# Kernel tuning notes

Measured on AMD Instinct MI355X. Metric: run time of the kernel, lower is better.

The kernel has to match this reference:

```python
import jax, jax.numpy as jnp
import numpy as np

# Fixed architecture constants from the source
B, T, D, V, L, H = 4096, 128, 64, 65, 3, 8
HD = D // H  # head_size = 8
DF = 4 * D   # 256


def _layernorm(x, g, b, eps=1e-5):
    mu = jnp.mean(x, axis=-1, keepdims=True)
    var = jnp.mean(jnp.square(x - mu), axis=-1, keepdims=True)
    return (x - mu) * jax.lax.rsqrt(var + eps) * g + b


def setup_inputs() -> dict:
    key = jax.random.key(0)
    ks = iter(jax.random.split(key, 64))
    s = 0.02
    n = lambda shape: jax.random.normal(next(ks), shape, dtype=jnp.float32) * s
    inp = {
        "tok_emb": n((V, D)),
        "pos_emb": n((T, D)),
        # per-block params stacked on leading layer dim L=3
        "ln1_g": jnp.ones((L, D), jnp.float32), "ln1_b": jnp.zeros((L, D), jnp.float32),
        "wq": n((L, D, D)), "wk": n((L, D, D)), "wv": n((L, D, D)),
        "wo": n((L, D, D)), "bo": jnp.zeros((L, D), jnp.float32),
        "ln2_g": jnp.ones((L, D), jnp.float32), "ln2_b": jnp.zeros((L, D), jnp.float32),
        "w1": n((L, D, DF)), "b1": jnp.zeros((L, DF), jnp.float32),
        "w2": n((L, DF, D)), "b2": jnp.zeros((L, D), jnp.float32),
        "lnf_g": jnp.ones((D,), jnp.float32), "lnf_b": jnp.zeros((D,), jnp.float32),
        "lm_w": n((D, V)), "lm_b": jnp.zeros((V,), jnp.float32),
        "idx": jax.random.randint(next(ks), (B, T), 0, V),
        "targets": jax.random.randint(next(ks), (B, T), 0, V),
    }
    return inp


def _forward(tok_emb, pos_emb, ln1_g, ln1_b, wq, wk, wv, wo, bo,
             ln2_g, ln2_b, w1, b1, w2, b2, lnf_g, lnf_b, lm_w, lm_b,
             idx, targets):
    b, t = idx.shape
    x = tok_emb[idx] + pos_emb[:t]  # [B,T,D]
    mask = jnp.tril(jnp.ones((t, t), bool))
    scale = 1.0 / np.sqrt(HD)
    for l in range(L):  # 3 structurally identical blocks (dropout = identity at eval)
        xn = _layernorm(x, ln1_g[l], ln1_b[l])
        # 8 per-head projections fused into one [D,D] matmul (concat along out dim)
        q = (xn @ wq[l]).reshape(b, t, H, HD)
        k = (xn @ wk[l]).reshape(b, t, H, HD)
        v = (xn @ wv[l]).reshape(b, t, H, HD)
        scores = jnp.einsum('bqhd,bkhd->bhqk', q, k) * scale
        scores = jnp.where(mask, scores, -jnp.inf)
        probs = jax.nn.softmax(scores, axis=-1)
        attn = jnp.einsum('bhqk,bkhd->bqhd', probs, v).reshape(b, t, D)
        x = x + attn @ wo[l] + bo[l]
        xn = _layernorm(x, ln2_g[l], ln2_b[l])
        x = x + jax.nn.relu(xn @ w1[l] + b1[l]) @ w2[l] + b2[l]
    x = _layernorm(x, lnf_g, lnf_b)
    logits = (x @ lm_w + lm_b).reshape(b * t, V)
    logp = jax.nn.log_softmax(logits, axis=-1)
    loss = -jnp.mean(jnp.take_along_axis(logp, targets.reshape(b * t, 1), axis=1))
    return logits, loss


def reference(tok_emb, pos_emb, ln1_g, ln1_b, wq, wk, wv, wo, bo,
              ln2_g, ln2_b, w1, b1, w2, b2, lnf_g, lnf_b, lm_w, lm_b,
              idx, targets):
    return _forward(tok_emb, pos_emb, ln1_g, ln1_b, wq, wk, wv, wo, bo,
                    ln2_g, ln2_b, w1, b1, w2, b2, lnf_g, lnf_b, lm_w, lm_b,
                    idx, targets)
```

## Files before the change

kernel.cpp:

```cpp
#include <hip/hip_runtime.h>
#include <hip/hip_bf16.h>

#define NB  4096
#define NT  128
#define ND  64
#define NV  65
#define NL  3
#define NH  8
#define NDF 256
#define NBT (NB*NT)

#define OFF_TOK   0
#define OFF_POS   4160
#define OFF_LN1G  12352
#define OFF_LN1B  12544
#define OFF_WQ    12736
#define OFF_WK    25024
#define OFF_WV    37312
#define OFF_WO    49600
#define OFF_BO    61888
#define OFF_LN2G  62080
#define OFF_LN2B  62272
#define OFF_W1    62464
#define OFF_B1    111616
#define OFF_W2    112384
#define OFF_B2    161536
#define OFF_LNFG  161728
#define OFF_LNFB  161792
#define OFF_LMW   161856
#define OFF_LMB   166016
#define CVT_TOTAL 166081
#define OFF_LOSS  166144
#define OFF_FLAG  166145

#define PKF       166148
#define PK_ELEMS  147456
#define NEED_WS   ((size_t)(PKF + PK_ELEMS) * 4)

typedef short s8v  __attribute__((ext_vector_type(8)));
typedef float f4v  __attribute__((ext_vector_type(4)));

struct CvtArgs { const void* p[19]; };

__device__ __forceinline__ unsigned short f2bf(float x) {
    unsigned int u = __float_as_uint(x);
    u = (u + 0x7fffu + ((u >> 16) & 1u)) >> 16;
    return (unsigned short)u;
}
__device__ __forceinline__ float bf2f(unsigned short h) {
    return __uint_as_float(((unsigned int)h) << 16);
}
__device__ __forceinline__ f4v mfma16(s8v a, s8v b, f4v c) {
    return __builtin_amdgcn_mfma_f32_16x16x32_bf16(a, b, c, 0, 0, 0);
}

__global__ void diag_fill(float* __restrict__ out, int n, float val) {
    int i = blockIdx.x * 256 + threadIdx.x;
    if (i < n) out[i] = val;
}

__global__ void detect_float(const unsigned short* __restrict__ tok,
                             int* __restrict__ flags) {
    int bad = 0;
    for (int i = threadIdx.x; i < 4096; i += 256) {
        float v = __uint_as_float(((unsigned int)tok[i]) << 16);
        if (!(fabsf(v) < 1000.f)) bad = 1;
    }
    if (bad) atomicOr(flags, 1);
}

__global__ void detect_int(const int* __restrict__ idx32,
                           int* __restrict__ flags) {
    int proven = 0;
    #pragma unroll
    for (int j = 0; j < 8; j++) {
        int slot = 2 * (threadIdx.x * 8 + j) + 1;
        if (idx32[slot] != 0) proven = 1;
    }
    if (proven) atomicOr(flags, 4);
}

__global__ void cvt_params(CvtArgs a, float* __restrict__ W,
                           const int* __restrict__ flags) {
    int tid = blockIdx.x * 256 + threadIdx.x;
    if (tid >= CVT_TOTAL) return;
    const int offs[20] = {0,4160,12352,12544,12736,25024,37312,49600,61888,
                          62080,62272,62464,111616,112384,161536,161728,
                          161792,161856,166016,166081};
    int s = 0;
    #pragma unroll
    for (int k = 1; k < 19; k++) s += (tid >= offs[k]);
    int local = tid - offs[s];
    if (*flags & 1) {
        W[tid] = ((const float*)a.p[s])[local];
    } else {
        unsigned int v = ((const unsigned short*)a.p[s])[local];
        W[tid] = __uint_as_float(v << 16);
    }
}

__global__ void pack_weights(const float* __restrict__ W,
                             unsigned short* __restrict__ pkw) {
    int p = blockIdx.x * 256 + threadIdx.x;
    if (p >= PK_ELEMS) return;
    int srcoff, K, N, perlay, local, ktbits;
    if (p < 49152) {
        int grp = p / 12288; local = p % 12288;
        srcoff = (grp == 0) ? OFF_WQ : (grp == 1) ? OFF_WK
               : (grp == 2) ? OFF_WV : OFF_WO;
        K = 64; N = 64; perlay = 4096; ktbits = 1;
    } else if (p < 98304) {
        local = p - 49152; srcoff = OFF_W1; K = 64; N = 256;
        perlay = 16384; ktbits = 1;
    } else {
        local = p - 98304; srcoff = OFF_W2; K = 256; N = 64;
        perlay = 16384; ktbits = 3;
    }
    int lay = local / perlay, rem = local % perlay;
    int t = rem >> 9, le = rem & 511, l = le >> 3, e = le & 7;
    int kt = t & ((1 << ktbits) - 1), nt = t >> ktbits;
    int row = kt * 32 + (l >> 4) * 8 + e;
    int col = nt * 16 + (l & 15);
    float v = W[srcoff + lay * K * N + row * N + col];
    unsigned short hi = f2bf(v);
    pkw[p] = hi;
    pkw[PK_ELEMS + p] = f2bf(v - bf2f(hi));
}

__global__ void mfma_probe(int* __restrict__ flags) {
    int l = threadIdx.x;
    s8v av, bv;
    int i = l & 15;
    #pragma unroll
    for (int e = 0; e < 8; e++) {
        int k = (l >> 4) * 8 + e;
        av[e] = (short)f2bf((float)(((i * 5 + k * 3) & 7) - 3));
        bv[e] = (short)f2bf((float)(((k * 7 + i * 11) & 7) - 4));
    }
    f4v c = {0.f, 0.f, 0.f, 0.f};
    c = mfma16(av, bv, c);
    int bad = 0;
    #pragma unroll
    for (int reg = 0; reg < 4; reg++) {
        int row = (l >> 4) * 4 + reg, col = l & 15;
        float exp = 0.f;
        for (int k = 0; k < 32; k++)
            exp += (float)(((row * 5 + k * 3) & 7) - 3) *
                   (float)(((k * 7 + col * 11) & 7) - 4);
        if (c[reg] != exp) bad = 1;
    }
    if (bad) atomicOr(flags, 8);
}

__device__ __forceinline__ void unpack8(uint4 u, float* f) {
    f[0] = __uint_as_float(u.x << 16); f[1] = __uint_as_float(u.x & 0xffff0000u);
    f[2] = __uint_as_float(u.y << 16); f[3] = __uint_as_float(u.y & 0xffff0000u);
    f[4] = __uint_as_float(u.z << 16); f[5] = __uint_as_float(u.z & 0xffff0000u);
    f[6] = __uint_as_float(u.w << 16); f[7] = __uint_as_float(u.w & 0xffff0000u);
}

__device__ __forceinline__ void ln_rm(const float (*src)[68], float (*dst)[68],
                                      const float* __restrict__ g,
                                      const float* __restrict__ bb, int tid) {
    int r = tid >> 3, q = tid & 7;
    int c0 = q * 8;
    float s = 0.f, s2 = 0.f;
    #pragma unroll
    for (int c = 0; c < 8; c++) { float v = src[r][c0 + c]; s += v; s2 += v * v; }
    s += __shfl_xor(s, 1);  s2 += __shfl_xor(s2, 1);
    s += __shfl_xor(s, 2);  s2 += __shfl_xor(s2, 2);
    s += __shfl_xor(s, 4);  s2 += __shfl_xor(s2, 4);
    float mu   = s  * (1.f / 64.f);
    float var  = s2 * (1.f / 64.f) - mu * mu;
    float rstd = rsqrtf(var + 1e-5f);
    #pragma unroll
    for (int c = 0; c < 8; c++) {
        int cc = c0 + c;
        dst[r][cc] = (src[r][cc] - mu) * rstd * g[cc] + bb[cc];
    }
}

__device__ __forceinline__ void ln_frag(const float (*src)[68],
        unsigned short* __restrict__ dhi, unsigned short* __restrict__ dlo,
        const float* __restrict__ g, const float* __restrict__ bb, int tid) {
    int r = tid >> 3, q = tid & 7, c0 = q * 8;
    float s = 0.f, s2 = 0.f;
    #pragma unroll
    for (int c = 0; c < 8; c++) { float v = src[r][c0 + c]; s += v; s2 += v * v; }
    s += __shfl_xor(s, 1);  s2 += __shfl_xor(s2, 1);
    s += __shfl_xor(s, 2);  s2 += __shfl_xor(s2, 2);
    s += __shfl_xor(s, 4);  s2 += __shfl_xor(s2, 4);
    float mu   = s  * (1.f / 64.f);
    float var  = s2 * (1.f / 64.f) - mu * mu;
    float rstd = rsqrtf(var + 1e-5f);
    unsigned uh[4], ul[4];
    #pragma unroll
    for (int c2 = 0; c2 < 4; c2++) {
        float y0 = (src[r][c0 + c2*2    ] - mu) * rstd * g[c0 + c2*2    ] + bb[c0 + c2*2    ];
        float y1 = (src[r][c0 + c2*2 + 1] - mu) * rstd * g[c0 + c2*2 + 1] + bb[c0 + c2*2 + 1];
        unsigned short h0 = f2bf(y0), h1 = f2bf(y1);
        uh[c2] = (unsigned)h0 | ((unsigned)h1 << 16);
        ul[c2] = (unsigned)f2bf(y0 - bf2f(h0)) | ((unsigned)f2bf(y1 - bf2f(h1)) << 16);
    }
    int di = (((r >> 4) * 2 + (q >> 2)) * 64 + (q & 3) * 16 + (r & 15)) * 8;
    *(uint4*)(dhi + di) = make_uint4(uh[0], uh[1], uh[2], uh[3]);
    *(uint4*)(dlo + di) = make_uint4(ul[0], ul[1], ul[2], ul[3]);
}

__device__ __forceinline__ void fma16(const float* xr, const float* wr, float& a) {
    float4 x0 = *(const float4*)(xr);
    float4 x1 = *(const float4*)(xr + 4);
    float4 x2 = *(const float4*)(xr + 8);
    float4 x3 = *(const float4*)(xr + 12);
    a = fmaf(x0.x, wr[0],  a); a = fmaf(x0.y, wr[1],  a);
    a = fmaf(x0.z, wr[2],  a); a = fmaf(x0.w, wr[3],  a);
    a = fmaf(x1.x, wr[4],  a); a = fmaf(x1.y, wr[5],  a);
    a = fmaf(x1.z, wr[6],  a); a = fmaf(x1.w, wr[7],  a);
    a = fmaf(x2.x, wr[8],  a); a = fmaf(x2.y, wr[9],  a);
    a = fmaf(x2.z, wr[10], a); a = fmaf(x2.w, wr[11], a);
    a = fmaf(x3.x, wr[12], a); a = fmaf(x3.y, wr[13], a);
    a = fmaf(x3.z, wr[14], a); a = fmaf(x3.w, wr[15], a);
}

__device__ void ln_scalar(const float* x, float* o,
                          const float* g, const float* bb) {
    float mu = 0.f;
    for (int i = 0; i < ND; i++) mu += x[i];
    mu *= (1.f / 64.f);
    float var = 0.f;
    for (int i = 0; i < ND; i++) { float d = x[i] - mu; var += d * d; }
    var *= (1.f / 64.f);
    float rstd = rsqrtf(var + 1e-5f);
    for (int i = 0; i < ND; i++) o[i] = (x[i] - mu) * rstd * g[i] + bb[i];
}

__global__ __launch_bounds__(1024, 4) void gpt_fwd(
    const float* __restrict__ W, const unsigned short* __restrict__ pkw,
    int usepk, const void* __restrict__ idxp, const void* __restrict__ tgtp,
    float* __restrict__ out, float* __restrict__ loss_acc,
    const int* __restrict__ flags)
{
    __shared__ alignas(16) float xs[NT][68];
    __shared__ alignas(16) unsigned char regB[34816];
    __shared__ alignas(16) unsigned char uni[65536];
    __shared__ float wsum[16];

    float (*xnR)[68] = (float (*)[68])regB;
    unsigned short* xah = (unsigned short*)regB;
    unsigned short* xal = (unsigned short*)(regB + 16384);
    unsigned short (*qs)[72] = (unsigned short (*)[72])(uni);
    unsigned short (*ks)[72] = (unsigned short (*)[72])(uni + 18432);
    unsigned short (*vs)[72] = (unsigned short (*)[72])(uni + 36864);
    unsigned short* ha = (unsigned short*)uni;
    unsigned short* hl = (unsigned short*)(uni + 32768);
    float (*hch)[264] = (float (*)[264])uni;

    const int tid  = threadIdx.x;
    const int lane = tid & 63;
    const int w    = tid >> 6;
    const int b    = blockIdx.x;
    const int fl   = *flags;
    const bool i64 = !(fl & 4);
    const bool use_mfma = usepk && !(fl & 8);
    const int*       idx32 = (const int*)idxp;
    const long long* idx64 = (const long long*)idxp;
    const int*       tgt32 = (const int*)tgtp;
    const long long* tgt64 = (const long long*)tgtp;

    for (int e = tid * 4; e < NT * ND; e += 4096) {
        int r = e >> 6, c = e & 63;
        int n = b * NT + r;
        int tok = i64 ? (int)idx64[n] : idx32[n];
        float4 te = *(const float4*)&W[OFF_TOK + tok * ND + c];
        float4 pe = *(const float4*)&W[OFF_POS + r * ND + c];
        float4 xv;
        xv.x = te.x + pe.x; xv.y = te.y + pe.y;
        xv.z = te.z + pe.z; xv.w = te.w + pe.w;
        *(float4*)&xs[r][c] = xv;
    }
    __syncthreads();

    if (use_mfma) {
        for (int lay = 0; lay < NL; lay++) {
            ln_frag(xs, xah, xal, W + OFF_LN1G + lay * 64, W + OFF_LN1B + lay * 64, tid);
            __syncthreads();

            {
                const unsigned short* pbase = pkw + lay * 4096;
                #pragma unroll 1
                for (int i = 0; i < 6; i++) {
                    int ft = w * 6 + i;
                    int mat = ft >> 5, mt = (ft >> 2) & 7, nt = ft & 3;
                    const unsigned short* pb = pbase + mat * 12288 + nt * 1024 + lane * 8;
                    f4v acc = {0.f, 0.f, 0.f, 0.f};
                    #pragma unroll
                    for (int kt = 0; kt < 2; kt++) {
                        s8v ah = *(const s8v*)(xah + ((mt * 2 + kt) * 64 + lane) * 8);
                        s8v al = *(const s8v*)(xal + ((mt * 2 + kt) * 64 + lane) * 8);
                        s8v bh = *(const s8v*)(pb + kt * 512);
                        s8v bl = *(const s8v*)(pb + PK_ELEMS + kt * 512);
                        acc = mfma16(ah, bh, acc);
                        acc = mfma16(ah, bl, acc);
                        acc = mfma16(al, bh, acc);
                    }
                    unsigned short (*dst)[72] = (mat == 0) ? qs : (mat == 1) ? ks : vs;
                    int row0 = mt * 16 + (lane >> 4) * 4, col = nt * 16 + (lane & 15);
                    dst[row0    ][col] = f2bf(acc[0]);
                    dst[row0 + 1][col] = f2bf(acc[1]);
                    dst[row0 + 2][col] = f2bf(acc[2]);
                    dst[row0 + 3][col] = f2bf(acc[3]);
                }
            }
            __syncthreads();

            {
                const int head = w & 7, hh = w >> 3;
                const int h8 = head * 8;
                const int r  = lane + hh * 64;
                const float scale = 0.35355339059327373f;
                float qv[8];
                uint4 qq = *(const uint4*)&qs[r][h8];
                unpack8(qq, qv);
                #pragma unroll
                for (int d = 0; d < 8; d++) qv[d] *= scale;
                float m = -1e30f, lsum = 0.f;
                float o[8] = {0, 0, 0, 0, 0, 0, 0, 0};
                for (int base = 0; base <= r; base += 8) {
                    float sc[8];
                    #pragma unroll
                    for (int t = 0; t < 8; t++) {
                        int kk = base + t; kk = kk > 127 ? 127 : kk;
                        uint4 kr = *(const uint4*)&ks[kk][h8];
                        float kf[8]; unpack8(kr, kf);
                        float s = 0.f;
                        #pragma unroll
                        for (int d = 0; d < 8; d++) s = fmaf(qv[d], kf[d], s);
                        sc[t] = (base + t <= r) ? s : -1e30f;
                    }
                    float cm = fmaxf(fmaxf(fmaxf(sc[0], sc[1]), fmaxf(sc[2], sc[3])),
                                     fmaxf(fmaxf(sc[4], sc[5]), fmaxf(sc[6], sc[7])));
                    float nm  = fmaxf(m, cm);
                    float fac = __expf(m - nm);
                    lsum *= fac;
                    #pragma unroll
                    for (int d = 0; d < 8; d++) o[d] *= fac;
                    #pragma unroll
                    for (int t = 0; t < 8; t++) {
                        float p = __expf(sc[t] - nm);
                        int kk = base + t; kk = kk > 127 ? 127 : kk;
                        uint4 vr = *(const uint4*)&vs[kk][h8];
                        float vf[8]; unpack8(vr, vf);
                        lsum += p;
                        #pragma unroll
                        for (int d = 0; d < 8; d++) o[d] = fmaf(p, vf[d], o[d]);
                    }
                    m = nm;
                }
                float inv = 1.f / lsum;
                float y[8];
                #pragma unroll
                for (int d = 0; d < 8; d++) y[d] = o[d] * inv;
                unsigned uh[4], ul[4];
                #pragma unroll
                for (int c2 = 0; c2 < 4; c2++) {
                    unsigned short h0 = f2bf(y[c2*2]), h1 = f2bf(y[c2*2+1]);
                    uh[c2] = (unsigned)h0 | ((unsigned)h1 << 16);
                    ul[c2] = (unsigned)f2bf(y[c2*2]   - bf2f(h0)) |
                             ((unsigned)f2bf(y[c2*2+1] - bf2f(h1)) << 16);
                }
                int di = (((r >> 4) * 2 + (head >> 2)) * 64 + (head & 3) * 16 + (r & 15)) * 8;
                *(uint4*)(xah + di) = make_uint4(uh[0], uh[1], uh[2], uh[3]);
                *(uint4*)(xal + di) = make_uint4(ul[0], ul[1], ul[2], ul[3]);
            }
            __syncthreads();

            {
                const unsigned short* pbase = pkw + 36864 + lay * 4096;
                const float* bo = W + OFF_BO + lay * 64;
                #pragma unroll 1
                for (int i = 0; i < 2; i++) {
                    int ft = w * 2 + i;
                    int mt = ft >> 2, nt = ft & 3;
                    const unsigned short* pb = pbase + nt * 1024 + lane * 8;
                    f4v acc = {0.f, 0.f, 0.f, 0.f};
                    #pragma unroll
                    for (int kt = 0; kt < 2; kt++) {
                        s8v ah = *(const s8v*)(xah + ((mt * 2 + kt) * 64 + lane) * 8);
                        s8v al = *(const s8v*)(xal + ((mt * 2 + kt) * 64 + lane) * 8);
                        s8v bh = *(const s8v*)(pb + kt * 512);
                        s8v bl = *(const s8v*)(pb + PK_ELEMS + kt * 512);
                        acc = mfma16(ah, bh, acc);
                        acc = mfma16(ah, bl, acc);
                        acc = mfma16(al, bh, acc);
                    }
                    int row0 = mt * 16 + (lane >> 4) * 4, col = nt * 16 + (lane & 15);
                    float bias = bo[col];
                    xs[row0    ][col] += acc[0] + bias;
                    xs[row0 + 1][col] += acc[1] + bias;
                    xs[row0 + 2][col] += acc[2] + bias;
                    xs[row0 + 3][col] += acc[3] + bias;
                }
            }
            __syncthreads();

            ln_frag(xs, xah, xal, W + OFF_LN2G + lay * 64, W + OFF_LN2B + lay * 64, tid);
            __syncthreads();

            for (int hh = 0; hh < 2; hh++) {
                {
                    const float* b1 = W + OFF_B1 + lay * 256;
                    #pragma unroll 1
                    for (int i = 0; i < 4; i++) {
                        int ft = w * 4 + i;
                        int mtl = ft >> 4, nt = ft & 15;
                        int mt = hh * 4 + mtl;
                        const unsigned short* pb = pkw + 49152 + lay * 16384 + nt * 1024 + lane * 8;
                        f4v acc = {0.f, 0.f, 0.f, 0.f};
                        #pragma unroll
                        for (int kt = 0; kt < 2; kt++) {
                            s8v ah = *(const s8v*)(xah + ((mt * 2 + kt) * 64 + lane) * 8);
                            s8v al = *(const s8v*)(xal + ((mt * 2 + kt) * 64 + lane) * 8);
                            s8v bh = *(const s8v*)(pb + kt * 512);
                            s8v bl = *(const s8v*)(pb + PK_ELEMS + kt * 512);
                            acc = mfma16(ah, bh, acc);
                            acc = mfma16(ah, bl, acc);
                            acc = mfma16(al, bh, acc);
                        }
                        int col = nt * 16 + (lane & 15);
                        float bias = b1[col];
                        int kt2 = col >> 5, q2 = (col >> 3) & 3, e2 = col & 7;
                        #pragma unroll
                        for (int i2 = 0; i2 < 4; i2++) {
                            int lr = mtl * 16 + (lane >> 4) * 4 + i2;
                            float hvv = fmaxf(acc[i2] + bias, 0.f);
                            int di = ((mtl * 8 + kt2) * 64 + q2 * 16 + (lr & 15)) * 8 + e2;
                            unsigned short hi = f2bf(hvv);
                            ha[di] = hi;
                            hl[di] = f2bf(hvv - bf2f(hi));
                        }
                    }
                }
                __syncthreads();
                {
                    const float* b2 = W + OFF_B2 + lay * 64;
                    int mtl = w >> 2, nt = w & 3;
                    const unsigned short* pb = pkw + 98304 + lay * 16384 + nt * 4096 + lane * 8;
                    f4v acc = {0.f, 0.f, 0.f, 0.f};
                    #pragma unroll 2
                    for (int kt = 0; kt < 8; kt++) {
                        s8v ah = *(const s8v*)(ha + ((mtl * 8 + kt) * 64 + lane) * 8);
                        s8v al = *(const s8v*)(hl + ((mtl * 8 + kt) * 64 + lane) * 8);
                        s8v bh = *(const s8v*)(pb + kt * 512);
                        s8v bl = *(const s8v*)(pb + PK_ELEMS + kt * 512);
                        acc = mfma16(ah, bh, acc);
                        acc = mfma16(ah, bl, acc);
                        acc = mfma16(al, bh, acc);
                    }
                    int row0 = hh * 64 + mtl * 16 + (lane >> 4) * 4, col = nt * 16 + (lane & 15);
                    float bias = b2[col];
                    xs[row0    ][col] += acc[0] + bias;
                    xs[row0 + 1][col] += acc[1] + bias;
                    xs[row0 + 2][col] += acc[2] + bias;
                    xs[row0 + 3][col] += acc[3] + bias;
                }
                __syncthreads();
            }
        }
        ln_rm(xs, xnR, W + OFF_LNFG, W + OFF_LNFB, tid);
        __syncthreads();
    } else {
        for (int lay = 0; lay < NL; lay++) {
            ln_rm(xs, xnR, W + OFF_LN1G + lay * 64, W + OFF_LN1B + lay * 64, tid);
            __syncthreads();
            {
                #pragma unroll 1
                for (int mmat = 0; mmat < 3; mmat++) {
                    const float* wm = W + (mmat == 0 ? OFF_WQ : (mmat == 1 ? OFF_WK : OFF_WV))
                                        + lay * ND * ND;
                    unsigned short (*dstp)[72] = (mmat == 0) ? qs : ((mmat == 1) ? ks : vs);
                    float acc[8];
                    #pragma unroll
                    for (int rr = 0; rr < 8; rr++) acc[rr] = 0.f;
                    #pragma unroll 1
                    for (int ih = 0; ih < 4; ih++) {
                        float wr[16];
                        #pragma unroll
                        for (int i = 0; i < 16; i++) wr[i] = wm[(ih * 16 + i) * ND + lane];
                        #pragma unroll
                        for (int rr = 0; rr < 8; rr++)
                            fma16(&xnR[w * 8 + rr][ih * 16], wr, acc[rr]);
                    }
                    #pragma unroll
                    for (int rr = 0; rr < 8; rr++)
                        dstp[w * 8 + rr][lane] = f2bf(acc[rr]);
                }
            }
            __syncthreads();
            {
                const int head = w & 7, hh = w >> 3;
                const int h8 = head * 8;
                const int r  = lane + hh * 64;
                const float scale = 0.35355339059327373f;
                float qv[8];
                uint4 qq = *(const uint4*)&qs[r][h8];
                unpack8(qq, qv);
                #pragma unroll
                for (int d = 0; d < 8; d++) qv[d] *= scale;
                float m = -1e30f, lsum = 0.f;
                float o[8] = {0, 0, 0, 0, 0, 0, 0, 0};
                for (int base = 0; base <= r; base += 8) {
                    float sc[8];
                    #pragma unroll
                    for (int t = 0; t < 8; t++) {
                        int kk = base + t; kk = kk > 127 ? 127 : kk;
                        uint4 kr = *(const uint4*)&ks[kk][h8];
                        float kf[8]; unpack8(kr, kf);
                        float s = 0.f;
                        #pragma unroll
                        for (int d = 0; d < 8; d++) s = fmaf(qv[d], kf[d], s);
                        sc[t] = (base + t <= r) ? s : -1e30f;
                    }
                    float cm = fmaxf(fmaxf(fmaxf(sc[0], sc[1]), fmaxf(sc[2], sc[3])),
                                     fmaxf(fmaxf(sc[4], sc[5]), fmaxf(sc[6], sc[7])));
                    float nm  = fmaxf(m, cm);
                    float fac = __expf(m - nm);
                    lsum *= fac;
                    #pragma unroll
                    for (int d = 0; d < 8; d++) o[d] *= fac;
                    #pragma unroll
                    for (int t = 0; t < 8; t++) {
                        float p = __expf(sc[t] - nm);
                        int kk = base + t; kk = kk > 127 ? 127 : kk;
                        uint4 vr = *(const uint4*)&vs[kk][h8];
                        float vf[8]; unpack8(vr, vf);
                        lsum += p;
                        #pragma unroll
                        for (int d = 0; d < 8; d++) o[d] = fmaf(p, vf[d], o[d]);
                    }
                    m = nm;
                }
                float inv = 1.f / lsum;
                #pragma unroll
                for (int d = 0; d < 8; d++) xnR[r][h8 + d] = o[d] * inv;
            }
            __syncthreads();
            {
                const float* wo = W + OFF_WO + lay * ND * ND;
                float acc[8];
                #pragma unroll
                for (int rr = 0; rr < 8; rr++) acc[rr] = W[OFF_BO + lay * ND + lane];
                #pragma unroll 1
                for (int ih = 0; ih < 4; ih++) {
                    float wr[16];
                    #pragma unroll
                    for (int i = 0; i < 16; i++) wr[i] = wo[(ih * 16 + i) * ND + lane];
                    #pragma unroll
                    for (int rr = 0; rr < 8; rr++)
                        fma16(&xnR[w * 8 + rr][ih * 16], wr, acc[rr]);
                }
                #pragma unroll
                for (int rr = 0; rr < 8; rr++)
                    xs[w * 8 + rr][lane] += acc[rr];
            }
            __syncthreads();
            ln_rm(xs, xnR, W + OFF_LN2G + lay * 64, W + OFF_LN2B + lay * 64, tid);
            __syncthreads();
            {
                const float* w1 = W + OFF_W1 + lay * ND * NDF;
                const float* w2 = W + OFF_W2 + lay * NDF * ND;
                const float* b1 = W + OFF_B1 + lay * NDF;
                const float* b2 = W + OFF_B2 + lay * ND;
                for (int ch = 0; ch < 4; ch++) {
                    int rbase = ch * 32;
                    {
                        int lr = tid >> 5;
                        int j0 = (tid & 31) * 8;
                        int r  = rbase + lr;
                        float4 ba  = *(const float4*)(b1 + j0);
                        float4 bb4 = *(const float4*)(b1 + j0 + 4);
                        float a0 = ba.x,  a1 = ba.y,  a2 = ba.z,  a3 = ba.w;
                        float a4 = bb4.x, a5 = bb4.y, a6 = bb4.z, a7 = bb4.w;
                        #pragma unroll 4
                        for (int i4 = 0; i4 < ND; i4 += 4) {
                            float4 xv = *(const float4*)&xnR[r][i4];
                            #pragma unroll
                            for (int s = 0; s < 4; s++) {
                                float xvs = (s == 0) ? xv.x : (s == 1) ? xv.y
                                          : (s == 2) ? xv.z : xv.w;
                                float4 wa = *(const float4*)(w1 + (i4 + s) * NDF + j0);
                                float4 wb = *(const float4*)(w1 + (i4 + s) * NDF + j0 + 4);
                                a0 = fmaf(xvs, wa.x, a0); a1 = fmaf(xvs, wa.y, a1);
                                a2 = fmaf(xvs, wa.z, a2); a3 = fmaf(xvs, wa.w, a3);
                                a4 = fmaf(xvs, wb.x, a4); a5 = fmaf(xvs, wb.y, a5);
                                a6 = fmaf(xvs, wb.z, a6); a7 = fmaf(xvs, wb.w, a7);
                            }
                        }
                        float4 h0, h1;
                        h0.x = fmaxf(a0, 0.f); h0.y = fmaxf(a1, 0.f);
                        h0.z = fmaxf(a2, 0.f); h0.w = fmaxf(a3, 0.f);
                        h1.x = fmaxf(a4, 0.f); h1.y = fmaxf(a5, 0.f);
                        h1.z = fmaxf(a6, 0.f); h1.w = fmaxf(a7, 0.f);
                        *(float4*)&hch[lr][j0]     = h0;
                        *(float4*)&hch[lr][j0 + 4] = h1;
                    }
                    __syncthreads();
                    {
                        int lr = tid >> 5;
                        int i0 = (tid & 31) * 2;
                        int r  = rbase + lr;
                        float a0 = 0.f, a1 = 0.f;
                        #pragma unroll 4
                        for (int j4 = 0; j4 < NDF; j4 += 4) {
                            float4 hv = *(const float4*)&hch[lr][j4];
                            #pragma unroll
                            for (int s = 0; s < 4; s++) {
                                float hvs = (s == 0) ? hv.x : (s == 1) ? hv.y
                                          : (s == 2) ? hv.z : hv.w;
                                float2 w2v = *(const float2*)(w2 + (j4 + s) * ND + i0);
                                a0 = fmaf(hvs, w2v.x, a0); a1 = fmaf(hvs, w2v.y, a1);
                            }
                        }
                        float2 bb2 = *(const float2*)(b2 + i0);
                        xs[r][i0]     += a0 + bb2.x;
                        xs[r][i0 + 1] += a1 + bb2.y;
                    }
                    __syncthreads();
                }
            }
        }
        ln_rm(xs, xnR, W + OFF_LNFG, W + OFF_LNFB, tid);
        __syncthreads();
    }

    {
        const float* lmw = W + OFF_LMW;
        float wacc = 0.f;
        for (int rr = 0; rr < 8; rr++) {
            int r = w * 8 + rr;
            float lg  = W[OFF_LMB + lane];
            float lg2 = W[OFF_LMB + 64];
            #pragma unroll 8
            for (int i = 0; i < ND; i++) {
                float xv = xnR[r][i];
                lg  = fmaf(xv, lmw[i * NV + lane], lg);
                lg2 = fmaf(xv, lmw[i * NV + 64],  lg2);
            }
            float M = lg;
            #pragma unroll
            for (int off = 32; off; off >>= 1) M = fmaxf(M, __shfl_xor(M, off));
            M = fmaxf(M, lg2);
            float ssum = __expf(lg - M);
            #pragma unroll
            for (int off = 32; off; off >>= 1) ssum += __shfl_xor(ssum, off);
            ssum += __expf(lg2 - M);
            float lse = M + logf(ssum);
            int row = b * NT + r;
            int tg  = i64 ? (int)tgt64[row] : tgt32[row];
            float lt = (tg < 64) ? __shfl(lg, tg) : lg2;
            wacc += lt - lse;
            out[row * NV + lane] = lg;
            if (lane == 0) out[row * NV + 64] = lg2;
        }
        if (lane == 0) wsum[w] = wacc;
        __syncthreads();
        if (tid == 0) {
            float t = 0.f;
            #pragma unroll
            for (int wv = 0; wv < 16; wv++) t += wsum[wv];
            atomicAdd(loss_acc, t);
        }
    }
    __syncthreads();

    if (b == 0 && tid == 0) {
        float x0[ND], xn0[ND], v0[ND], h0[NDF];
        int tok0 = i64 ? (int)idx64[0] : idx32[0];
        for (int c = 0; c < ND; c++)
            x0[c] = W[OFF_TOK + tok0 * ND + c] + W[OFF_POS + c];
        for (int l = 0; l < NL; l++) {
            ln_scalar(x0, xn0, W + OFF_LN1G + l * ND, W + OFF_LN1B + l * ND);
            for (int c = 0; c < ND; c++) {
                float a = 0.f;
                for (int i = 0; i < ND; i++)
                    a += xn0[i] * W[OFF_WV + l * ND * ND + i * ND + c];
                v0[c] = a;
            }
            for (int c = 0; c < ND; c++) {
                float a = W[OFF_BO + l * ND + c];
                for (int i = 0; i < ND; i++)
                    a += v0[i] * W[OFF_WO + l * ND * ND + i * ND + c];
                x0[c] += a;
            }
            ln_scalar(x0, xn0, W + OFF_LN2G + l * ND, W + OFF_LN2B + l * ND);
            for (int j = 0; j < NDF; j++) {
                float a = W[OFF_B1 + l * NDF + j];
                for (int i = 0; i < ND; i++)
                    a += xn0[i] * W[OFF_W1 + l * ND * NDF + i * NDF + j];
                h0[j] = fmaxf(a, 0.f);
            }
            for (int c = 0; c < ND; c++) {
                float a = W[OFF_B2 + l * ND + c];
                for (int j = 0; j < NDF; j++)
                    a += h0[j] * W[OFF_W2 + l * NDF * ND + j * ND + c];
                x0[c] += a;
            }
        }
        ln_scalar(x0, xn0, W + OFF_LNFG, W + OFF_LNFB);
        bool bad = false;
        for (int v = 0; v < NV; v++) {
            float lg = W[OFF_LMB + v];
            for (int i = 0; i < ND; i++)
                lg += xn0[i] * W[OFF_LMW + i * NV + v];
            if (!(fabsf(out[v] - lg) <= 0.05f)) bad = true;
        }
        if (bad) out[0] = 100.0f;
    }
}

__global__ void finalize_loss(const float* __restrict__ acc,
                              float* __restrict__ out) {
    out[NBT * NV] = -acc[0] * (1.f / (float)NBT);
}

extern "C" void kernel_launch(void* const* d_in, const int* in_sizes, int n_in,
                              void* d_out, int out_size, void* d_ws, size_t ws_size,
                              hipStream_t stream)
{
    static const int want[21] = {4160, 8192, 192, 192, 12288, 12288, 12288,
                                 12288, 192, 192, 192, 49152, 768, 49152, 192,
                                 64, 64, 4160, 65, 524288, 524288};
    int diag = 0;
    if (n_in != 21) diag = 3;
    else for (int i = 0; i < 21; i++) if (in_sizes[i] != want[i]) { diag = 3; break; }
    if (!diag && out_size != NBT * NV + 1) diag = 4;
    if (!diag && ws_size < (size_t)(OFF_FLAG + 1) * 4) diag = 5;
    if (diag) {
        diag_fill<<<(out_size + 255) / 256, 256, 0, stream>>>(
            (float*)d_out, out_size, (float)diag);
        return;
    }

    float* W = (float*)d_ws;
    float* loss_acc = W + OFF_LOSS;
    int*   flags    = (int*)(W + OFF_FLAG);
    hipMemsetAsync(W + OFF_LOSS, 0, 2 * sizeof(float), stream);

    detect_float<<<1, 256, 0, stream>>>((const unsigned short*)d_in[0], flags);
    detect_int  <<<1, 256, 0, stream>>>((const int*)d_in[19], flags);
    mfma_probe  <<<1, 64,  0, stream>>>(flags);

    CvtArgs a;
    for (int i = 0; i < 19; i++) a.p[i] = d_in[i];
    cvt_params<<<(CVT_TOTAL + 255) / 256, 256, 0, stream>>>(a, W, flags);

    int usepk = (ws_size >= NEED_WS) ? 1 : 0;
    unsigned short* pkw = (unsigned short*)(W + PKF);
    if (usepk)
        pack_weights<<<(PK_ELEMS + 255) / 256, 256, 0, stream>>>(W, pkw);

    gpt_fwd<<<NB, 1024, 0, stream>>>(W, pkw, usepk, d_in[19], d_in[20],
                                     (float*)d_out, loss_acc, flags);
    finalize_loss<<<1, 1, 0, stream>>>(loss_acc, (float*)d_out);
}
```

Measured before the change: 2.776 ms.

## Compute causal attention with MFMA tiles instead of scalar online softmax

Replaces the per-thread scalar online-softmax attention loop with 16x16x16 bf16 MFMA tiles for QK^T and PV. Q, K and V are written head-major (V pre-transposed), with the softmax scale folded into Q, and zero-padded K=8 head dimensions fed through a shared zero block. Softmax runs over registers with cross-lane shuffles, and probabilities are staged through per-wave LDS scratch. This cuts the scalar FMA and LDS read cost of attention, but adds padding waste, extra bf16 rounding of probabilities, and more LDS traffic for the P transpose.

```diff
diff --git a/kernel.cpp b/kernel.cpp
--- a/kernel.cpp
+++ b/kernel.cpp
@@ -243,11 +243,15 @@
     __shared__ alignas(16) float xs[NT][68];
     __shared__ alignas(16) unsigned char regB[34816];
     __shared__ alignas(16) unsigned char uni[65536];
+    __shared__ alignas(16) unsigned short zblk[8];
     __shared__ float wsum[16];
 
     float (*xnR)[68] = (float (*)[68])regB;
     unsigned short* xah = (unsigned short*)regB;
     unsigned short* xal = (unsigned short*)(regB + 16384);
+    unsigned short* q_lds = (unsigned short*)uni;
+    unsigned short* k_lds = (unsigned short*)(uni + 16384);
+    unsigned short* vb    = (unsigned short*)(uni + 32768);
     unsigned short (*qs)[72] = (unsigned short (*)[72])(uni);
     unsigned short (*ks)[72] = (unsigned short (*)[72])(uni + 18432);
     unsigned short (*vs)[72] = (unsigned short (*)[72])(uni + 36864);
@@ -267,6 +271,8 @@
     const int*       tgt32 = (const int*)tgtp;
     const long long* tgt64 = (const long long*)tgtp;
 
+    if (tid < 8) zblk[tid] = 0;
+
     for (int e = tid * 4; e < NT * ND; e += 4096) {
         int r = e >> 6, c = e & 63;
         int n = b * NT + r;
@@ -303,74 +309,125 @@
                         acc = mfma16(ah, bl, acc);
                         acc = mfma16(al, bh, acc);
                     }
-                    unsigned short (*dst)[72] = (mat == 0) ? qs : (mat == 1) ? ks : vs;
-                    int row0 = mt * 16 + (lane >> 4) * 4, col = nt * 16 + (lane & 15);
-                    dst[row0    ][col] = f2bf(acc[0]);
-                    dst[row0 + 1][col] = f2bf(acc[1]);
-                    dst[row0 + 2][col] = f2bf(acc[2]);
-                    dst[row0 + 3][col] = f2bf(acc[3]);
+                    int row0 = mt * 16 + (lane >> 4) * 4;
+                    int fullcol = nt * 16 + (lane & 15);
+                    int head = fullcol >> 3, dim = fullcol & 7;
+                    if (mat == 0) {
+                        #pragma unroll
+                        for (int i2 = 0; i2 < 4; i2++)
+                            q_lds[(head * 128 + row0 + i2) * 8 + dim] =
+                                f2bf(acc[i2] * 0.35355339059327373f);
+                    } else if (mat == 1) {
+                        #pragma unroll
+                        for (int i2 = 0; i2 < 4; i2++)
+                            k_lds[(head * 128 + row0 + i2) * 8 + dim] = f2bf(acc[i2]);
+                    } else {
+                        #pragma unroll
+                        for (int i2 = 0; i2 < 4; i2++) {
+                            int key = row0 + i2;
+                            vb[((((head * 4) + (key >> 5)) * 4 + ((key >> 3) & 3)) * 8
+                                + dim) * 8 + (key & 7)] = f2bf(acc[i2]);
+                        }
+                    }
                 }
             }
             __syncthreads();
 
             {
-                const int head = w & 7, hh = w >> 3;
-                const int h8 = head * 8;
-                const int r  = lane + hh * 64;
-                const float scale = 0.35355339059327373f;
-                float qv[8];
-                uint4 qq = *(const uint4*)&qs[r][h8];
-                unpack8(qq, qv);
-                #pragma unroll
-                for (int d = 0; d < 8; d++) qv[d] *= scale;
-                float m = -1e30f, lsum = 0.f;
-                float o[8] = {0, 0, 0, 0, 0, 0, 0, 0};
-                for (int base = 0; base <= r; base += 8) {
-                    float sc[8];
-                    #pragma unroll
-                    for (int t = 0; t < 8; t++) {
-                        int kk = base + t; kk = kk > 127 ? 127 : kk;
-                        uint4 kr = *(const uint4*)&ks[kk][h8];
-                        float kf[8]; unpack8(kr, kf);
-                        float s = 0.f;
-                        #pragma unroll
-                        for (int d = 0; d < 8; d++) s = fmaf(qv[d], kf[d], s);
-                        sc[t] = (base + t <= r) ? s : -1e30f;
-                    }
-                    float cm = fmaxf(fmaxf(fmaxf(sc[0], sc[1]), fmaxf(sc[2], sc[3])),
-                                     fmaxf(fmaxf(sc[4], sc[5]), fmaxf(sc[6], sc[7])));
-                    float nm  = fmaxf(m, cm);
-                    float fac = __expf(m - nm);
-                    lsum *= fac;
-                    #pragma unroll
-                    for (int d = 0; d < 8; d++) o[d] *= fac;
-                    #pragma unroll
-                    for (int t = 0; t < 8; t++) {
-                        float p = __expf(sc[t] - nm);
-                        int kk = base + t; kk = kk > 127 ? 127 : kk;
-                        uint4 vr = *(const uint4*)&vs[kk][h8];
-                        float vf[8]; unpack8(vr, vf);
-                        lsum += p;
-                        #pragma unroll
-                        for (int d = 0; d < 8; d++) o[d] = fmaf(p, vf[d], o[d]);
-                    }
-                    m = nm;
+                unsigned short* pscr = (unsigned short*)(uni + 49152) + w * 512;
+                const int cl = lane & 15, g = lane >> 4;
+                #pragma unroll 1
+                for (int ti = 0; ti < 4; ti++) {
+                    int t = w + ti * 16;
+                    int mt = t >> 3, head = t & 7;
+                    const unsigned short* qsrc = (lane < 16)
+                        ? q_lds + (head * 128 + mt * 16 + cl) * 8 : zblk;
+                    s8v qa = *(const s8v*)qsrc;
+                    f4v sv[8];
+                    #pragma unroll
+                    for (int nt = 0; nt < 8; nt++) {
+                        sv[nt] = (f4v){0.f, 0.f, 0.f, 0.f};
+                        if (nt <= mt) {
+                            const unsigned short* ksrc = (lane < 16)
+                                ? k_lds + (head * 128 + nt * 16 + cl) * 8 : zblk;
+                            s8v kb = *(const s8v*)ksrc;
+                            sv[nt] = mfma16(qa, kb, sv[nt]);
+                            if (nt == mt) {
+                                #pragma unroll
+                                for (int i2 = 0; i2 < 4; i2++)
+                                    sv[nt][i2] = (cl <= g * 4 + i2) ? sv[nt][i2] : -1e30f;
+                            }
+                        }
+                    }
+                    float mx[4] = {-1e30f, -1e30f, -1e30f, -1e30f};
+                    #pragma unroll
+                    for (int nt = 0; nt < 8; nt++)
+                        if (nt <= mt) {
+                            #pragma unroll
+                            for (int i2 = 0; i2 < 4; i2++)
+                                mx[i2] = fmaxf(mx[i2], sv[nt][i2]);
+                        }
+                    #pragma unroll
+                    for (int i2 = 0; i2 < 4; i2++) {
+                        mx[i2] = fmaxf(mx[i2], __shfl_xor(mx[i2], 1));
+                        mx[i2] = fmaxf(mx[i2], __shfl_xor(mx[i2], 2));
+                        mx[i2] = fmaxf(mx[i2], __shfl_xor(mx[i2], 4));
+                        mx[i2] = fmaxf(mx[i2], __shfl_xor(mx[i2], 8));
+                    }
+                    float sm[4] = {0.f, 0.f, 0.f, 0.f};
+                    #pragma unroll
+                    for (int nt = 0; nt < 8; nt++)
+                        if (nt <= mt) {
+                            #pragma unroll
+                            for (int i2 = 0; i2 < 4; i2++) {
+                                float p = __expf(sv[nt][i2] - mx[i2]);
+                                sv[nt][i2] = p;
+                                sm[i2] += p;
+                            }
+                        }
+                    #pragma unroll
+                    for (int i2 = 0; i2 < 4; i2++) {
+                        sm[i2] += __shfl_xor(sm[i2], 1);
+                        sm[i2] += __shfl_xor(sm[i2], 2);
+                        sm[i2] += __shfl_xor(sm[i2], 4);
+                        sm[i2] += __shfl_xor(sm[i2], 8);
+                    }
+                    float inv[4];
+                    #pragma unroll
+                    for (int i2 = 0; i2 < 4; i2++) inv[i2] = 1.f / sm[i2];
+                    f4v o = {0.f, 0.f, 0.f, 0.f};
+                    #pragma unroll
+                    for (int kt = 0; kt < 4; kt++) {
+                        if (kt <= (mt >> 1)) {
+                            #pragma unroll
+                            for (int s2 = 0; s2 < 2; s2++) {
+                                int nt = kt * 2 + s2;
+                                #pragma unroll
+                                for (int i2 = 0; i2 < 4; i2++) {
+                                    float pv = (nt <= mt) ? sv[nt][i2] * inv[i2] : 0.f;
+                                    pscr[(g * 4 + i2) * 32 + s2 * 16 + cl] = f2bf(pv);
+                                }
+                            }
+                            s8v pa = *(const s8v*)(pscr + cl * 32 + g * 8);
+                            const unsigned short* vsrc = (cl < 8)
+                                ? vb + ((((head * 4) + kt) * 4 + g) * 8 + cl) * 8 : zblk;
+                            s8v vf = *(const s8v*)vsrc;
+                            o = mfma16(pa, vf, o);
+                        }
+                    }
+                    if (cl < 8) {
+                        #pragma unroll
+                        for (int i2 = 0; i2 < 4; i2++) {
+                            int r = mt * 16 + g * 4 + i2;
+                            float y = o[i2];
+                            unsigned short h = f2bf(y);
+                            int di = (((r >> 4) * 2 + (head >> 2)) * 64
+                                      + (head & 3) * 16 + (r & 15)) * 8 + cl;
+                            xah[di] = h;
+                            xal[di] = f2bf(y - bf2f(h));
+                        }
+                    }
                 }
-                float inv = 1.f / lsum;
-                float y[8];
-                #pragma unroll
-                for (int d = 0; d < 8; d++) y[d] = o[d] * inv;
-                unsigned uh[4], ul[4];
-                #pragma unroll
-                for (int c2 = 0; c2 < 4; c2++) {
-                    unsigned short h0 = f2bf(y[c2*2]), h1 = f2bf(y[c2*2+1]);
-                    uh[c2] = (unsigned)h0 | ((unsigned)h1 << 16);
-                    ul[c2] = (unsigned)f2bf(y[c2*2]   - bf2f(h0)) |
-                             ((unsigned)f2bf(y[c2*2+1] - bf2f(h1)) << 16);
-                }
-                int di = (((r >> 4) * 2 + (head >> 2)) * 64 + (head & 3) * 16 + (r & 15)) * 8;
-                *(uint4*)(xah + di) = make_uint4(uh[0], uh[1], uh[2], uh[3]);
-                *(uint4*)(xal + di) = make_uint4(ul[0], ul[1], ul[2], ul[3]);
             }
             __syncthreads();
 
```

New measurement: 2.466 ms. 11.2% less time.
